# Performance work log

Measured on AMD Instinct MI355X. Metric: run time of the kernel, lower is better.

## Reference

```python
import jax, jax.numpy as jnp
import numpy as np

B, N, EMB, HID, CODE, FEAT, L = 8, 96, 768, 384, 192, 768, 2
NEG = 1e30  # mask_logic constant


def _gru(x, h, Wih, Whh, bih, bhh):
    # torch.nn.GRUCell math; gate order r, z, n
    gi = x @ Wih.T + bih
    gh = h @ Whh.T + bhh
    ir, iz, inn = jnp.split(gi, 3, axis=-1)
    hr, hz, hn = jnp.split(gh, 3, axis=-1)
    r = jax.nn.sigmoid(ir + hr)
    z = jax.nn.sigmoid(iz + hz)
    n = jnp.tanh(inn + r * hn)
    return (1.0 - z) * n + z * h


def _node0(Hl, gc, gp):
    # node 0: C = gru_c(x, 0); P = gru_p(0, x); H1 = C + P
    x0 = Hl[:, 0]
    z0 = jnp.zeros_like(x0)
    h0 = _gru(x0, z0, *gc) + _gru(z0, x0, *gp)
    b, n, d = Hl.shape
    return jnp.zeros((b, n, d), Hl.dtype).at[:, 0].set(h0)


def _dag_scan(Hl, s_mask, aux, Wr0, Wr1, gc, gp, get_w):
    # sequential DAG recurrence: node i attends over nodes < i of the CURRENT layer's outputs
    b, n, d = Hl.shape
    buf0 = _node0(Hl, gc, gp)
    pos = jnp.arange(n)

    def step(buf, inp):
        i, q, s_row, aux_row = inp
        valid = pos < i                                  # growing history slice [:i]
        w = get_w(buf, q, aux_row, valid)                # (B,N), zero for j >= i
        s = s_row[:, :, None]
        V = (buf @ Wr0.T) * s + (buf @ Wr1.T) * (1.0 - s)  # speaker-relation values
        M = jnp.einsum('bn,bnd->bd', w, V)
        hn = _gru(q, M, *gc) + _gru(M, q, *gp)           # C + P
        return buf.at[:, i].set(hn), w

    xs = (jnp.arange(1, n),
          jnp.swapaxes(Hl[:, 1:], 0, 1),
          jnp.swapaxes(s_mask[:, 1:], 0, 1),
          jnp.swapaxes(aux[:, 1:], 0, 1))
    buf, ws = jax.lax.scan(step, buf0, xs)
    return buf, jnp.swapaxes(ws, 0, 1)  # H1 (B,N,D), attn rows 1..N-1 (B,N-1,N)


def _mlp(x, W0, b0, W1, b1):
    # out_mlp with mlp_layers=1 (dropout is identity in eval mode)
    return jax.nn.relu(x @ W0.T + b0) @ W1.T + b1


def _forward(features, adj, s_mask, s_mask_onehot,
             enc_fc1_W, enc_fc1_b, enc_gat_w, enc_gat_b, enc_Wr0, enc_Wr1,
             enc_gruc_Wih, enc_gruc_Whh, enc_gruc_bih, enc_gruc_bhh,
             enc_grup_Wih, enc_grup_Whh, enc_grup_bih, enc_grup_bhh,
             enc_mlp_W0, enc_mlp_b0, enc_mlp_W1, enc_mlp_b1,
             dec_fc1_W, dec_fc1_b, dec_Wr0, dec_Wr1,
             dec_gruc_Wih, dec_gruc_Whh, dec_gruc_bih, dec_gruc_bhh,
             dec_grup_Wih, dec_grup_Whh, dec_grup_bih, dec_grup_bhh,
             dec_mlp_W0, dec_mlp_b0, dec_mlp_W1, dec_mlp_b1,
             lengths):
    b, n, _ = features.shape
    I = jnp.broadcast_to(jnp.eye(n, dtype=features.dtype), (b, n, n))
    # ----- encoder -----
    Hs = [jax.nn.relu(features @ enc_fc1_W.T + enc_fc1_b)]
    adjB_list = [jnp.zeros((b, 1, n), features.dtype)]
    for l in range(L):
        gc = (enc_gruc_Wih[l], enc_gruc_Whh[l], enc_gruc_bih[l], enc_gruc_bhh[l])
        gp = (enc_grup_Wih[l], enc_grup_Whh[l], enc_grup_bih[l], enc_grup_bhh[l])
        wq, wk, gb = enc_gat_w[l, :HID], enc_gat_w[l, HID:], enc_gat_b[l]

        def get_w(buf, q, adj_row, valid, wq=wq, wk=wk, gb=gb):
            # GAT_encoder: alpha = Linear([q; K]) masked by adj over history (mask_logic)
            alpha = buf @ wk + (q @ wq)[:, None] + gb
            alpha = alpha - (1.0 - adj_row) * NEG
            alpha = jnp.where(valid[None, :], alpha, -jnp.inf)
            return jax.nn.softmax(alpha, axis=-1)

        H1, ws = _dag_scan(Hs[l], s_mask, adj, enc_Wr0[l], enc_Wr1[l], gc, gp, get_w)
        Hs.append(H1)
        # row 0 of adjB is zeros; rows 1..N-1 are zero-padded attention weights
        adjB_list.append(jnp.concatenate([jnp.zeros((b, 1, n), features.dtype), ws], axis=1))
    fU = _mlp(jnp.concatenate(Hs, axis=-1), enc_mlp_W0, enc_mlp_b0, enc_mlp_W1, enc_mlp_b1)
    # ----- decoder -----
    Hs = [jax.nn.relu(fU @ dec_fc1_W.T + dec_fc1_b)]
    for l in range(L):
        gc = (dec_gruc_Wih[l], dec_gruc_Whh[l], dec_gruc_bih[l], dec_gruc_bhh[l])
        gp = (dec_grup_Wih[l], dec_grup_Whh[l], dec_grup_bih[l], dec_grup_bhh[l])
        b_inv = jnp.linalg.solve(I, I - adjB_list[l + 1])

        def get_w(buf, q, w_row, valid):
            # GNN_decoder: uses b_inv[:, i, :i] directly as gather weights
            return jnp.where(valid[None, :], w_row, 0.0)

        H1, _ = _dag_scan(Hs[l], s_mask, b_inv, dec_Wr0[l], dec_Wr1[l], gc, gp, get_w)
        Hs.append(H1)
    logits = _mlp(jnp.concatenate(Hs, axis=-1), dec_mlp_W0, dec_mlp_b0, dec_mlp_W1, dec_mlp_b1)
    feature_map = jnp.linalg.solve(I, I - adjB_list[2])
    return logits, feature_map


def setup_inputs() -> dict:
    key = jax.random.key(0)
    ks = iter(jax.random.split(key, 48))

    def rn(*shape):
        return jax.random.normal(next(ks), shape, jnp.float32) * 0.05

    return dict(
        features=jax.random.normal(next(ks), (B, N, EMB), jnp.float32),
        adj=jax.random.randint(next(ks), (B, N, N), 0, 2).astype(jnp.float32),
        s_mask=jax.random.randint(next(ks), (B, N, N), 0, 2).astype(jnp.float32),
        s_mask_onehot=jnp.zeros((B, N, N, 2), jnp.float32),
        lengths=jax.random.randint(next(ks), (B,), 1, N),
        enc_fc1_W=rn(HID, EMB), enc_fc1_b=rn(HID),
        enc_gat_w=rn(L, 2 * HID), enc_gat_b=rn(L),
        enc_Wr0=rn(L, HID, HID), enc_Wr1=rn(L, HID, HID),
        enc_gruc_Wih=rn(L, 3 * HID, HID), enc_gruc_Whh=rn(L, 3 * HID, HID),
        enc_gruc_bih=rn(L, 3 * HID), enc_gruc_bhh=rn(L, 3 * HID),
        enc_grup_Wih=rn(L, 3 * HID, HID), enc_grup_Whh=rn(L, 3 * HID, HID),
        enc_grup_bih=rn(L, 3 * HID), enc_grup_bhh=rn(L, 3 * HID),
        enc_mlp_W0=rn(HID, (L + 1) * HID), enc_mlp_b0=rn(HID),
        enc_mlp_W1=rn(CODE, HID), enc_mlp_b1=rn(CODE),
        dec_fc1_W=rn(HID, CODE), dec_fc1_b=rn(HID),
        dec_Wr0=rn(L, HID, HID), dec_Wr1=rn(L, HID, HID),
        dec_gruc_Wih=rn(L, 3 * HID, HID), dec_gruc_Whh=rn(L, 3 * HID, HID),
        dec_gruc_bih=rn(L, 3 * HID), dec_gruc_bhh=rn(L, 3 * HID),
        dec_grup_Wih=rn(L, 3 * HID, HID), dec_grup_Whh=rn(L, 3 * HID, HID),
        dec_grup_bih=rn(L, 3 * HID), dec_grup_bhh=rn(L, 3 * HID),
        dec_mlp_W0=rn(HID, (L + 1) * HID), dec_mlp_b0=rn(HID),
        dec_mlp_W1=rn(FEAT, HID), dec_mlp_b1=rn(FEAT),
    )


def reference(features, adj, s_mask, s_mask_onehot, lengths,
              enc_fc1_W, enc_fc1_b, enc_gat_w, enc_gat_b, enc_Wr0, enc_Wr1,
              enc_gruc_Wih, enc_gruc_Whh, enc_gruc_bih, enc_gruc_bhh,
              enc_grup_Wih, enc_grup_Whh, enc_grup_bih, enc_grup_bhh,
              enc_mlp_W0, enc_mlp_b0, enc_mlp_W1, enc_mlp_b1,
              dec_fc1_W, dec_fc1_b, dec_Wr0, dec_Wr1,
              dec_gruc_Wih, dec_gruc_Whh, dec_gruc_bih, dec_gruc_bhh,
              dec_grup_Wih, dec_grup_Whh, dec_grup_bih, dec_grup_bhh,
              dec_mlp_W0, dec_mlp_b0, dec_mlp_W1, dec_mlp_b1):
    return _forward(features, adj, s_mask, s_mask_onehot,
                    enc_fc1_W, enc_fc1_b, enc_gat_w, enc_gat_b, enc_Wr0, enc_Wr1,
                    enc_gruc_Wih, enc_gruc_Whh, enc_gruc_bih, enc_gruc_bhh,
                    enc_grup_Wih, enc_grup_Whh, enc_grup_bih, enc_grup_bhh,
                    enc_mlp_W0, enc_mlp_b0, enc_mlp_W1, enc_mlp_b1,
                    dec_fc1_W, dec_fc1_b, dec_Wr0, dec_Wr1,
                    dec_gruc_Wih, dec_gruc_Whh, dec_gruc_bih, dec_gruc_bhh,
                    dec_grup_Wih, dec_grup_Whh, dec_grup_bih, dec_grup_bhh,
                    dec_mlp_W0, dec_mlp_b0, dec_mlp_W1, dec_mlp_b1,
                    lengths)
```

## Files before the change

kernel.cpp:

```cpp
#include <hip/hip_runtime.h>
#include <math.h>

#define B_    8
#define N_    96
#define EMB_  768
#define HID_  384
#define GID_  1152
#define CONC_ 1152
#define CODE_ 192
#define FEAT_ 768
#define NSL_  64
#define SD_   6
#define NRW_  42

__device__ __forceinline__ float sigf(float x) { return 1.0f / (1.0f + expf(-x)); }

__device__ __forceinline__ void atstf(float* p, float v) {
  __hip_atomic_store(p, v, __ATOMIC_RELAXED, __HIP_MEMORY_SCOPE_AGENT);
}
__device__ __forceinline__ float atldf(const float* p) {
  return __hip_atomic_load((float*)p, __ATOMIC_RELAXED, __HIP_MEMORY_SCOPE_AGENT);
}
__device__ __forceinline__ float dot4(float4 a, float4 b) {
  return fmaf(a.x, b.x, fmaf(a.y, b.y, fmaf(a.z, b.z, a.w * b.w)));
}

template<int RELU>
__global__ __launch_bounds__(256)
void gemm_bias(const float* __restrict__ A, int lda,
               const float* __restrict__ W,
               const float* __restrict__ bias,
               float* __restrict__ C, int ldc, int K)
{
  __shared__ float As[16][68];
  __shared__ float Bs[16][68];
  const int tid = threadIdx.x;
  const int m0 = blockIdx.y * 64;
  const int n0 = blockIdx.x * 64;
  const int lr = tid >> 2;
  const int lc = (tid & 3) * 4;
  const int ty = tid >> 4, tx = tid & 15;
  float acc[4][4] = {};
  for (int k0 = 0; k0 < K; k0 += 16) {
    float4 a4 = *(const float4*)(A + (size_t)(m0 + lr) * lda + k0 + lc);
    float4 b4 = *(const float4*)(W + (size_t)(n0 + lr) * K + k0 + lc);
    As[lc+0][lr] = a4.x; As[lc+1][lr] = a4.y; As[lc+2][lr] = a4.z; As[lc+3][lr] = a4.w;
    Bs[lc+0][lr] = b4.x; Bs[lc+1][lr] = b4.y; Bs[lc+2][lr] = b4.z; Bs[lc+3][lr] = b4.w;
    __syncthreads();
#pragma unroll
    for (int k = 0; k < 16; ++k) {
      float av[4], bv[4];
#pragma unroll
      for (int i = 0; i < 4; ++i) av[i] = As[k][ty*4+i];
#pragma unroll
      for (int j = 0; j < 4; ++j) bv[j] = Bs[k][tx*4+j];
#pragma unroll
      for (int i = 0; i < 4; ++i)
#pragma unroll
        for (int j = 0; j < 4; ++j) acc[i][j] = fmaf(av[i], bv[j], acc[i][j]);
    }
    __syncthreads();
  }
#pragma unroll
  for (int i = 0; i < 4; ++i) {
    int m = m0 + ty*4 + i;
#pragma unroll
    for (int j = 0; j < 4; ++j) {
      int n = n0 + tx*4 + j;
      float v = acc[i][j] + bias[n];
      if (RELU) v = fmaxf(v, 0.0f);
      C[(size_t)m * ldc + n] = v;
    }
  }
}

__global__ __launch_bounds__(256)
void prod_kernel(const float* __restrict__ Ac, const float* __restrict__ Ap,
                 const float* __restrict__ W0, const float* __restrict__ W1,
                 float* __restrict__ G)
{
  const float* A = (blockIdx.z < 2) ? Ac : Ap;
  const float* W = (blockIdx.z & 1) ? W1 : W0;
  float* C = G + (size_t)blockIdx.z * GID_ * HID_;
  __shared__ float As[16][68];
  __shared__ float Bs[16][68];
  const int tid = threadIdx.x;
  const int m0 = blockIdx.y * 64;
  const int n0 = blockIdx.x * 64;
  const int lr = tid >> 2;
  const int lc = (tid & 3) * 4;
  const int lr2 = tid & 63, kq = tid >> 6;
  const int ty = tid >> 4, tx = tid & 15;
  float acc[4][4] = {};
  for (int k0 = 0; k0 < HID_; k0 += 16) {
    float4 a4 = *(const float4*)(A + (size_t)(m0 + lr) * HID_ + k0 + lc);
    As[lc+0][lr] = a4.x; As[lc+1][lr] = a4.y; As[lc+2][lr] = a4.z; As[lc+3][lr] = a4.w;
#pragma unroll
    for (int u = 0; u < 4; ++u) {
      int kl = kq * 4 + u;
      Bs[kl][lr2] = W[(size_t)(k0 + kl) * HID_ + n0 + lr2];
    }
    __syncthreads();
#pragma unroll
    for (int k = 0; k < 16; ++k) {
      float av[4], bv[4];
#pragma unroll
      for (int i = 0; i < 4; ++i) av[i] = As[k][ty*4+i];
#pragma unroll
      for (int j = 0; j < 4; ++j) bv[j] = Bs[k][tx*4+j];
#pragma unroll
      for (int i = 0; i < 4; ++i)
#pragma unroll
        for (int j = 0; j < 4; ++j) acc[i][j] = fmaf(av[i], bv[j], acc[i][j]);
    }
    __syncthreads();
  }
#pragma unroll
  for (int i = 0; i < 4; ++i)
#pragma unroll
    for (int j = 0; j < 4; ++j)
      C[(size_t)(m0 + ty*4 + i) * HID_ + n0 + tx*4 + j] = acc[i][j];
}

struct ScanP {
  const float* Hl;
  float*       bufC;
  float*       hnX;
  const float* G;
  const float* GIc;
  const float* GHp;
  const float* bhhc;
  const float* bihp;
  const float* Wr0;
  const float* Wr1;
  const float* wk;
  const float* mask;
  const float* smask;
  float*       adjB;
};

template<int ENC>
__global__ __launch_bounds__(256, 2)
void scan_kernel(ScanP p)
{
  const int tid  = threadIdx.x;
  const int b    = blockIdx.x >> 6;
  const int sl   = blockIdx.x & 63;
  const int j0   = sl * SD_;
  const int team = tid >> 4, lane = tid & 15;

  __shared__ __align__(16) float stage[HID_];
  __shared__ float ws0[N_], ws1[N_], s_sm[N_];
  __shared__ float alpha[N_];
  __shared__ float dots[48];
  __shared__ float red4[4];
  __shared__ float sh_aknew;
  __shared__ float PA[NRW_ * 97];
  __shared__ float PB[NRW_ * 97];

  for (int k = tid; k < NRW_ * 97; k += 256) { PA[k] = 0.f; PB[k] = 0.f; }

  float4 wAr[3][6], wBr[3][6];
#pragma unroll
  for (int u = 0; u < 3; ++u) {
    const int r = team + 16 * u;
    const float *Aptr, *Bptr;
    if (r < 36) {
      const int g = r / 6, jl = r % 6;
      const size_t off = (size_t)((g % 3) * HID_ + j0 + jl) * HID_;
      const float* base = p.G + (g < 3 ? 0 : 2) * (size_t)GID_ * HID_;
      Aptr = base + off;
      Bptr = base + (size_t)GID_ * HID_ + off;
    } else if (r < 42) {
      const int jl = r - 36;
      Aptr = p.Wr0 + (size_t)(j0 + jl) * HID_;
      Bptr = p.Wr1 + (size_t)(j0 + jl) * HID_;
    } else if (r == 42 && ENC) {
      Aptr = p.wk; Bptr = p.wk;
    } else {
      Aptr = p.Wr0; Bptr = p.Wr1;
    }
#pragma unroll
    for (int m = 0; m < 6; ++m) {
      wAr[u][m] = ((const float4*)Aptr)[lane + 16*m];
      wBr[u][m] = ((const float4*)Bptr)[lane + 16*m];
    }
  }
  float bh0=0, bh1=0, bh2=0, bi0=0, bi1=0, bi2=0;
  if (tid < SD_) {
    int j = j0 + tid;
    bh0 = p.bhhc[j]; bh1 = p.bhhc[HID_ + j]; bh2 = p.bhhc[2*HID_ + j];
    bi0 = p.bihp[j]; bi1 = p.bihp[HID_ + j]; bi2 = p.bihp[2*HID_ + j];
  }

#define BULK_STAGE(SRC)                                                      \
  do {                                                                       \
    if (tid < NSL_) {                                                        \
      const float* f_ = (SRC) + tid * SD_;                                   \
      while (__float_as_uint(atldf(f_)) == 0xFFFFFFFFu) {}                   \
    }                                                                        \
    __syncthreads();                                                         \
    {                                                                        \
      float v0 = atldf((SRC) + tid);                                         \
      while (__float_as_uint(v0) == 0xFFFFFFFFu) v0 = atldf((SRC) + tid);    \
      stage[tid] = v0;                                                       \
      if (tid < HID_ - 256) {                                                \
        float v1 = atldf((SRC) + 256 + tid);                                 \
        while (__float_as_uint(v1) == 0xFFFFFFFFu)                           \
          v1 = atldf((SRC) + 256 + tid);                                     \
        stage[256 + tid] = v1;                                               \
      }                                                                      \
    }                                                                        \
    __syncthreads();                                                         \
  } while (0)

  if (tid < SD_) {
    int j = j0 + tid;
    const float* gi = p.GIc + (size_t)(b * N_) * GID_;
    const float* gh = p.GHp + (size_t)(b * N_) * GID_;
    float rc = sigf(gi[j] + bh0);
    float zc = sigf(gi[HID_ + j] + bh1);
    float nc = tanhf(gi[2*HID_ + j] + rc * bh2);
    float outc = (1.0f - zc) * nc;
    float rp = sigf(bi0 + gh[j]);
    float zp = sigf(bi1 + gh[HID_ + j]);
    float np = tanhf(bi2 + rp * gh[2*HID_ + j]);
    float x0 = p.Hl[(size_t)(b * N_) * CONC_ + j];
    float h0 = outc + (1.0f - zp) * np + zp * x0;
    p.bufC[(size_t)(b * N_) * CONC_ + j] = h0;
    atstf(&p.hnX[(size_t)(b * N_) * HID_ + j], h0);
  }
  __syncthreads();

  for (int i = 1; i < N_; ++i) {
    float pf_gi0=0, pf_gi1=0, pf_gi2=0, pf_gh0=0, pf_gh1=0, pf_gh2=0, pf_q=0;
    if (tid < SD_) {
      int j = j0 + tid;
      const float* gi = p.GIc + ((size_t)b * N_ + i) * GID_;
      const float* gh = p.GHp + ((size_t)b * N_ + i) * GID_;
      pf_gi0 = gi[j]; pf_gi1 = gi[HID_ + j]; pf_gi2 = gi[2*HID_ + j];
      pf_gh0 = gh[j]; pf_gh1 = gh[HID_ + j]; pf_gh2 = gh[2*HID_ + j];
      pf_q   = p.Hl[((size_t)b * N_ + i) * CONC_ + j];
    }
    float pf_mrow = 0.0f;
    if (tid < N_) {
      pf_mrow = p.mask[((size_t)b * N_ + i) * N_ + tid];
      s_sm[tid] = p.smask[((size_t)b * N_ + i) * N_ + tid];
    }

    const float* srcH = p.hnX + (size_t)(b * N_ + (i - 1)) * HID_;
    BULK_STAGE(srcH);
    const float4* st4 = (const float4*)stage;
    float4 hreg[6];
#pragma unroll
    for (int m = 0; m < 6; ++m) hreg[m] = st4[lane + 16*m];

#pragma unroll
    for (int u = 0; u < 3; ++u) {
      const int r = team + 16 * u;
      float a = 0.f, bv = 0.f;
#pragma unroll
      for (int m = 0; m < 6; ++m) {
        a  += dot4(wAr[u][m], hreg[m]);
        bv += dot4(wBr[u][m], hreg[m]);
      }
#pragma unroll
      for (int mm = 8; mm; mm >>= 1) {
        a  += __shfl_xor(a, mm);
        bv += __shfl_xor(bv, mm);
      }
      if (lane == 0) {
        if (r < NRW_) { PA[r * 97 + (i - 1)] = a; PB[r * 97 + (i - 1)] = bv; }
        else if (ENC && r == 42) sh_aknew = a;
      }
    }
    __syncthreads();

    if (ENC) {
      if (tid == 0) alpha[i - 1] = sh_aknew;
      float av = -3.0e38f;
      if (tid < i) {
        float ak = (tid == i - 1) ? sh_aknew : alpha[tid];
        av = ak - (1.0f - pf_mrow) * 1e30f;
      }
      float v = av;
#pragma unroll
      for (int m = 32; m; m >>= 1) v = fmaxf(v, __shfl_xor(v, m));
      if ((tid & 63) == 0) red4[tid >> 6] = v;
      __syncthreads();
      float mx = fmaxf(fmaxf(red4[0], red4[1]), fmaxf(red4[2], red4[3]));
      __syncthreads();
      float e = (tid < i) ? expf(av - mx) : 0.0f;
      v = e;
#pragma unroll
      for (int m = 32; m; m >>= 1) v += __shfl_xor(v, m);
      if ((tid & 63) == 0) red4[tid >> 6] = v;
      __syncthreads();
      float ssum = red4[0] + red4[1] + red4[2] + red4[3];
      if (tid < N_) {
        float w = (tid < i) ? e / ssum : 0.0f;
        float sv = s_sm[tid];
        ws0[tid] = w * sv;
        ws1[tid] = w - w * sv;
        if (sl == 0) p.adjB[((size_t)b * N_ + i) * N_ + tid] = w;
      }
      __syncthreads();
    } else {
      if (tid < N_) {
        float w = (tid < i) ? -pf_mrow : 0.0f;
        float sv = s_sm[tid];
        ws0[tid] = w * sv;
        ws1[tid] = w - w * sv;
      }
      __syncthreads();
    }

    {
      float wsr0[6], wsr1[6];
#pragma unroll
      for (int k = 0; k < 6; ++k) {
        wsr0[k] = ws0[lane + 16*k];
        wsr1[k] = ws1[lane + 16*k];
      }
#pragma unroll
      for (int u = 0; u < 3; ++u) {
        const int r = team + 16 * u;
        if (r < NRW_) {
          float acc = 0.f;
#pragma unroll
          for (int k = 0; k < 6; ++k) {
            int n = lane + 16*k;
            acc = fmaf(wsr0[k], PA[r * 97 + n], fmaf(wsr1[k], PB[r * 97 + n], acc));
          }
#pragma unroll
          for (int mm = 8; mm; mm >>= 1) acc += __shfl_xor(acc, mm);
          if (lane == 0) dots[r] = acc;
        }
      }
    }
    __syncthreads();

    if (tid < SD_) {
      int j = j0 + tid;
      float Mj = dots[36 + tid];
      float rc = sigf(pf_gi0 + dots[tid] + bh0);
      float zc = sigf(pf_gi1 + dots[6 + tid] + bh1);
      float nc = tanhf(pf_gi2 + rc * (dots[12 + tid] + bh2));
      float outc = (1.0f - zc) * nc + zc * Mj;
      float rp = sigf(dots[18 + tid] + bi0 + pf_gh0);
      float zp = sigf(dots[24 + tid] + bi1 + pf_gh1);
      float np = tanhf(dots[30 + tid] + bi2 + rp * pf_gh2);
      float hv = outc + (1.0f - zp) * np + zp * pf_q;
      p.bufC[((size_t)b * N_ + i) * CONC_ + j] = hv;
      atstf(&p.hnX[((size_t)b * N_ + i) * HID_ + j], hv);
    }
    __syncthreads();
  }
#undef BULK_STAGE
}

__global__ __launch_bounds__(256)
void fmap_kernel(const float* __restrict__ adjB2, float* __restrict__ out)
{
  int idx = blockIdx.x * 256 + threadIdx.x;
  if (idx < B_ * N_ * N_) {
    int j = idx % N_;
    int i = (idx / N_) % N_;
    float a = (i == 0) ? 0.0f : adjB2[idx];
    out[idx] = ((i == j) ? 1.0f : 0.0f) - a;
  }
}

extern "C" void kernel_launch(void* const* d_in, const int* in_sizes, int n_in,
                              void* d_out, int out_size, void* d_ws, size_t ws_size,
                              hipStream_t stream)
{
  (void)in_sizes; (void)n_in; (void)out_size; (void)ws_size;
  const float* features     = (const float*)d_in[0];
  const float* adj          = (const float*)d_in[1];
  const float* s_mask       = (const float*)d_in[2];
  const float* enc_fc1_W    = (const float*)d_in[5];
  const float* enc_fc1_b    = (const float*)d_in[6];
  const float* enc_gat_w    = (const float*)d_in[7];
  const float* enc_Wr0      = (const float*)d_in[9];
  const float* enc_Wr1      = (const float*)d_in[10];
  const float* enc_gruc_Wih = (const float*)d_in[11];
  const float* enc_gruc_Whh = (const float*)d_in[12];
  const float* enc_gruc_bih = (const float*)d_in[13];
  const float* enc_gruc_bhh = (const float*)d_in[14];
  const float* enc_grup_Wih = (const float*)d_in[15];
  const float* enc_grup_Whh = (const float*)d_in[16];
  const float* enc_grup_bih = (const float*)d_in[17];
  const float* enc_grup_bhh = (const float*)d_in[18];
  const float* enc_mlp_W0   = (const float*)d_in[19];
  const float* enc_mlp_b0   = (const float*)d_in[20];
  const float* enc_mlp_W1   = (const float*)d_in[21];
  const float* enc_mlp_b1   = (const float*)d_in[22];
  const float* dec_fc1_W    = (const float*)d_in[23];
  const float* dec_fc1_b    = (const float*)d_in[24];
  const float* dec_Wr0      = (const float*)d_in[25];
  const float* dec_Wr1      = (const float*)d_in[26];
  const float* dec_gruc_Wih = (const float*)d_in[27];
  const float* dec_gruc_Whh = (const float*)d_in[28];
  const float* dec_gruc_bih = (const float*)d_in[29];
  const float* dec_gruc_bhh = (const float*)d_in[30];
  const float* dec_grup_Wih = (const float*)d_in[31];
  const float* dec_grup_Whh = (const float*)d_in[32];
  const float* dec_grup_bih = (const float*)d_in[33];
  const float* dec_grup_bhh = (const float*)d_in[34];
  const float* dec_mlp_W0   = (const float*)d_in[35];
  const float* dec_mlp_b0   = (const float*)d_in[36];
  const float* dec_mlp_W1   = (const float*)d_in[37];
  const float* dec_mlp_b1   = (const float*)d_in[38];

  float* ws = (float*)d_ws;
  size_t o = 0;
  float* Hse   = ws + o; o += (size_t)B_ * N_ * CONC_;
  float* Hsd   = ws + o; o += (size_t)B_ * N_ * CONC_;
  float* GIc   = ws + o; o += (size_t)B_ * N_ * GID_;
  float* GHp   = ws + o; o += (size_t)B_ * N_ * GID_;
  float* adjB1 = ws + o; o += (size_t)B_ * N_ * N_;
  float* adjB2 = ws + o; o += (size_t)B_ * N_ * N_;
  float* fU    = ws + o; o += (size_t)B_ * N_ * CODE_;
  float* Tmp   = ws + o; o += (size_t)B_ * N_ * HID_;
  float* hnX   = ws + o; o += (size_t)B_ * N_ * HID_;
  float* Gbuf  = ws + o; o += (size_t)4 * GID_ * HID_;
  const size_t hn_bytes = (size_t)B_ * N_ * HID_ * sizeof(float);

  const dim3 blk(256);
  float* logits = (float*)d_out;
  float* fmap   = (float*)d_out + (size_t)B_ * N_ * FEAT_;

  gemm_bias<1><<<dim3(6, 12), blk, 0, stream>>>(features, EMB_, enc_fc1_W, enc_fc1_b,
                                                Hse, CONC_, EMB_);
  for (int l = 0; l < 2; ++l) {
    const float* Hl = Hse + l * HID_;
    gemm_bias<0><<<dim3(18, 12), blk, 0, stream>>>(Hl, CONC_,
        enc_gruc_Wih + (size_t)l * GID_ * HID_, enc_gruc_bih + l * GID_, GIc, GID_, HID_);
    gemm_bias<0><<<dim3(18, 12), blk, 0, stream>>>(Hl, CONC_,
        enc_grup_Whh + (size_t)l * GID_ * HID_, enc_grup_bhh + l * GID_, GHp, GID_, HID_);
    prod_kernel<<<dim3(6, 18, 4), blk, 0, stream>>>(
        enc_gruc_Whh + (size_t)l * GID_ * HID_, enc_grup_Wih + (size_t)l * GID_ * HID_,
        enc_Wr0 + (size_t)l * HID_ * HID_, enc_Wr1 + (size_t)l * HID_ * HID_, Gbuf);
    hipMemsetAsync(hnX, 0xFF, hn_bytes, stream);
    ScanP p;
    p.Hl = Hl; p.bufC = Hse + (l + 1) * HID_;
    p.hnX = hnX; p.G = Gbuf;
    p.GIc = GIc; p.GHp = GHp;
    p.bhhc = enc_gruc_bhh + l * GID_;
    p.bihp = enc_grup_bih + l * GID_;
    p.Wr0 = enc_Wr0 + (size_t)l * HID_ * HID_;
    p.Wr1 = enc_Wr1 + (size_t)l * HID_ * HID_;
    p.wk = enc_gat_w + l * 2 * HID_ + HID_;
    p.mask = adj; p.smask = s_mask;
    p.adjB = (l == 0) ? adjB1 : adjB2;
    scan_kernel<1><<<dim3(512), blk, 0, stream>>>(p);
  }
  gemm_bias<1><<<dim3(6, 12), blk, 0, stream>>>(Hse, CONC_, enc_mlp_W0, enc_mlp_b0,
                                                Tmp, HID_, CONC_);
  gemm_bias<0><<<dim3(3, 12), blk, 0, stream>>>(Tmp, HID_, enc_mlp_W1, enc_mlp_b1,
                                                fU, CODE_, HID_);
  gemm_bias<1><<<dim3(6, 12), blk, 0, stream>>>(fU, CODE_, dec_fc1_W, dec_fc1_b,
                                                Hsd, CONC_, CODE_);
  for (int l = 0; l < 2; ++l) {
    const float* Hl = Hsd + l * HID_;
    gemm_bias<0><<<dim3(18, 12), blk, 0, stream>>>(Hl, CONC_,
        dec_gruc_Wih + (size_t)l * GID_ * HID_, dec_gruc_bih + l * GID_, GIc, GID_, HID_);
    gemm_bias<0><<<dim3(18, 12), blk, 0, stream>>>(Hl, CONC_,
        dec_grup_Whh + (size_t)l * GID_ * HID_, dec_grup_bhh + l * GID_, GHp, GID_, HID_);
    prod_kernel<<<dim3(6, 18, 4), blk, 0, stream>>>(
        dec_gruc_Whh + (size_t)l * GID_ * HID_, dec_grup_Wih + (size_t)l * GID_ * HID_,
        dec_Wr0 + (size_t)l * HID_ * HID_, dec_Wr1 + (size_t)l * HID_ * HID_, Gbuf);
    hipMemsetAsync(hnX, 0xFF, hn_bytes, stream);
    ScanP p;
    p.Hl = Hl; p.bufC = Hsd + (l + 1) * HID_;
    p.hnX = hnX; p.G = Gbuf;
    p.GIc = GIc; p.GHp = GHp;
    p.bhhc = dec_gruc_bhh + l * GID_;
    p.bihp = dec_grup_bih + l * GID_;
    p.Wr0 = dec_Wr0 + (size_t)l * HID_ * HID_;
    p.Wr1 = dec_Wr1 + (size_t)l * HID_ * HID_;
    p.wk = nullptr;
    p.mask = (l == 0) ? adjB1 : adjB2;
    p.smask = s_mask;
    p.adjB = nullptr;
    scan_kernel<0><<<dim3(512), blk, 0, stream>>>(p);
  }
  gemm_bias<1><<<dim3(6, 12), blk, 0, stream>>>(Hsd, CONC_, dec_mlp_W0, dec_mlp_b0,
                                                Tmp, HID_, CONC_);
  gemm_bias<0><<<dim3(12, 12), blk, 0, stream>>>(Tmp, HID_, dec_mlp_W1, dec_mlp_b1,
                                                 logits, FEAT_, HID_);
  fmap_kernel<<<dim3((B_ * N_ * N_ + 255) / 256), blk, 0, stream>>>(adjB2, fmap);
}
```

Measured before the change: 1.961 ms.

## Precompute partial softmax and history dot before waiting on the newest node

The scan step is restructured so the softmax over the already known history and the weighted PA/PB reduction run before the wait for node i-1's hidden state. The newest entry is then folded in with an online-softmax rescale from the freshly computed projections. This takes that work off the cross-block dependency chain. The change also drops the flag-polling phase in favour of direct spin loads with s_sleep, remaps block indices so slices are spread across the grid, and pins weight registers with inline asm. The risks are numerical differences from the online rescale, extra register pressure, and correctness of the remapping, which depends on the grid size.

```diff
diff --git a/kernel.cpp b/kernel.cpp
--- a/kernel.cpp
+++ b/kernel.cpp
@@ -24,6 +24,7 @@
 __device__ __forceinline__ float dot4(float4 a, float4 b) {
   return fmaf(a.x, b.x, fmaf(a.y, b.y, fmaf(a.z, b.z, a.w * b.w)));
 }
+#define PIN4(v4) asm volatile("" : "+v"((v4).x), "+v"((v4).y), "+v"((v4).z), "+v"((v4).w))
 
 template<int RELU>
 __global__ __launch_bounds__(256)
@@ -144,16 +145,17 @@
 void scan_kernel(ScanP p)
 {
   const int tid  = threadIdx.x;
-  const int b    = blockIdx.x >> 6;
-  const int sl   = blockIdx.x & 63;
+  const int bid  = blockIdx.x;
+  const int b    = (bid >> 3) & 7;
+  const int sl   = ((bid & 7) << 3) | (bid >> 6);
   const int j0   = sl * SD_;
   const int team = tid >> 4, lane = tid & 15;
 
   __shared__ __align__(16) float stage[HID_];
-  __shared__ float ws0[N_], ws1[N_], s_sm[N_];
+  __shared__ float Ew0[N_], Ew1[N_], s_sm[N_], msk[N_];
   __shared__ float alpha[N_];
   __shared__ float dots[48];
-  __shared__ float red4[4];
+  __shared__ float red4a[4], red4b[4];
   __shared__ float sh_aknew;
   __shared__ float PA[NRW_ * 97];
   __shared__ float PB[NRW_ * 97];
@@ -186,6 +188,11 @@
       wBr[u][m] = ((const float4*)Bptr)[lane + 16*m];
     }
   }
+#pragma unroll
+  for (int u = 0; u < 3; ++u)
+#pragma unroll
+    for (int m = 0; m < 6; ++m) { PIN4(wAr[u][m]); PIN4(wBr[u][m]); }
+
   float bh0=0, bh1=0, bh2=0, bi0=0, bi1=0, bi2=0;
   if (tid < SD_) {
     int j = j0 + tid;
@@ -195,21 +202,19 @@
 
 #define BULK_STAGE(SRC)                                                      \
   do {                                                                       \
-    if (tid < NSL_) {                                                        \
-      const float* f_ = (SRC) + tid * SD_;                                   \
-      while (__float_as_uint(atldf(f_)) == 0xFFFFFFFFu) {}                   \
+    float v0 = atldf((SRC) + tid);                                           \
+    while (__float_as_uint(v0) == 0xFFFFFFFFu) {                             \
+      __builtin_amdgcn_s_sleep(2);                                           \
+      v0 = atldf((SRC) + tid);                                               \
     }                                                                        \
-    __syncthreads();                                                         \
-    {                                                                        \
-      float v0 = atldf((SRC) + tid);                                         \
-      while (__float_as_uint(v0) == 0xFFFFFFFFu) v0 = atldf((SRC) + tid);    \
-      stage[tid] = v0;                                                       \
-      if (tid < HID_ - 256) {                                                \
-        float v1 = atldf((SRC) + 256 + tid);                                 \
-        while (__float_as_uint(v1) == 0xFFFFFFFFu)                           \
-          v1 = atldf((SRC) + 256 + tid);                                     \
-        stage[256 + tid] = v1;                                               \
+    stage[tid] = v0;                                                         \
+    if (tid < HID_ - 256) {                                                  \
+      float v1 = atldf((SRC) + 256 + tid);                                   \
+      while (__float_as_uint(v1) == 0xFFFFFFFFu) {                           \
+        __builtin_amdgcn_s_sleep(2);                                         \
+        v1 = atldf((SRC) + 256 + tid);                                       \
       }                                                                      \
+      stage[256 + tid] = v1;                                                 \
     }                                                                        \
     __syncthreads();                                                         \
   } while (0)
@@ -242,10 +247,59 @@
       pf_gh0 = gh[j]; pf_gh1 = gh[HID_ + j]; pf_gh2 = gh[2*HID_ + j];
       pf_q   = p.Hl[((size_t)b * N_ + i) * CONC_ + j];
     }
-    float pf_mrow = 0.0f;
+    float mr = 0.f, sv_ = 0.f;
     if (tid < N_) {
-      pf_mrow = p.mask[((size_t)b * N_ + i) * N_ + tid];
-      s_sm[tid] = p.smask[((size_t)b * N_ + i) * N_ + tid];
+      mr  = p.mask[((size_t)b * N_ + i) * N_ + tid];
+      sv_ = p.smask[((size_t)b * N_ + i) * N_ + tid];
+      msk[tid] = mr; s_sm[tid] = sv_;
+    }
+    float f_mx = 0.f, f_se = 0.f;
+    if (ENC) {
+      float av = -3.0e38f;
+      if (tid < i - 1) av = alpha[tid] - (1.0f - mr) * 1e30f;
+      float v = av;
+#pragma unroll
+      for (int m = 32; m; m >>= 1) v = fmaxf(v, __shfl_xor(v, m));
+      if ((tid & 63) == 0) red4a[tid >> 6] = v;
+      __syncthreads();
+      f_mx = fmaxf(fmaxf(red4a[0], red4a[1]), fmaxf(red4a[2], red4a[3]));
+      float e = (tid < i - 1) ? expf(av - f_mx) : 0.0f;
+      v = e;
+#pragma unroll
+      for (int m = 32; m; m >>= 1) v += __shfl_xor(v, m);
+      if ((tid & 63) == 0) red4b[tid >> 6] = v;
+      if (tid < N_) { Ew0[tid] = e * sv_; Ew1[tid] = e - e * sv_; }
+      __syncthreads();
+      f_se = red4b[0] + red4b[1] + red4b[2] + red4b[3];
+    } else {
+      if (tid < N_) {
+        float w = (tid < i - 1) ? -mr : 0.0f;
+        Ew0[tid] = w * sv_; Ew1[tid] = w - w * sv_;
+      }
+      __syncthreads();
+    }
+
+    float er0[6], er1[6];
+#pragma unroll
+    for (int k = 0; k < 6; ++k) {
+      er0[k] = Ew0[lane + 16*k];
+      er1[k] = Ew1[lane + 16*k];
+    }
+    float sa_keep[3] = {0.f, 0.f, 0.f};
+#pragma unroll
+    for (int u = 0; u < 3; ++u) {
+      const int r = team + 16 * u;
+      if (r < NRW_) {
+        float acc = 0.f;
+#pragma unroll
+        for (int k = 0; k < 6; ++k) {
+          int n = lane + 16*k;
+          acc = fmaf(er0[k], PA[r * 97 + n], fmaf(er1[k], PB[r * 97 + n], acc));
+        }
+#pragma unroll
+        for (int mm = 8; mm; mm >>= 1) acc += __shfl_xor(acc, mm);
+        sa_keep[u] = acc;
+      }
     }
 
     const float* srcH = p.hnX + (size_t)(b * N_ + (i - 1)) * HID_;
@@ -255,6 +309,7 @@
 #pragma unroll
     for (int m = 0; m < 6; ++m) hreg[m] = st4[lane + 16*m];
 
+    float a_keep[3], b_keep[3];
 #pragma unroll
     for (int u = 0; u < 3; ++u) {
       const int r = team + 16 * u;
@@ -269,6 +324,7 @@
         a  += __shfl_xor(a, mm);
         bv += __shfl_xor(bv, mm);
       }
+      a_keep[u] = a; b_keep[u] = bv;
       if (lane == 0) {
         if (r < NRW_) { PA[r * 97 + (i - 1)] = a; PB[r * 97 + (i - 1)] = bv; }
         else if (ENC && r == 42) sh_aknew = a;
@@ -276,68 +332,26 @@
     }
     __syncthreads();
 
+    float c_scale, c_elast, c_inv;
     if (ENC) {
-      if (tid == 0) alpha[i - 1] = sh_aknew;
-      float av = -3.0e38f;
-      if (tid < i) {
-        float ak = (tid == i - 1) ? sh_aknew : alpha[tid];
-        av = ak - (1.0f - pf_mrow) * 1e30f;
-      }
-      float v = av;
-#pragma unroll
-      for (int m = 32; m; m >>= 1) v = fmaxf(v, __shfl_xor(v, m));
-      if ((tid & 63) == 0) red4[tid >> 6] = v;
-      __syncthreads();
-      float mx = fmaxf(fmaxf(red4[0], red4[1]), fmaxf(red4[2], red4[3]));
-      __syncthreads();
-      float e = (tid < i) ? expf(av - mx) : 0.0f;
-      v = e;
-#pragma unroll
-      for (int m = 32; m; m >>= 1) v += __shfl_xor(v, m);
-      if ((tid & 63) == 0) red4[tid >> 6] = v;
-      __syncthreads();
-      float ssum = red4[0] + red4[1] + red4[2] + red4[3];
-      if (tid < N_) {
-        float w = (tid < i) ? e / ssum : 0.0f;
-        float sv = s_sm[tid];
-        ws0[tid] = w * sv;
-        ws1[tid] = w - w * sv;
-        if (sl == 0) p.adjB[((size_t)b * N_ + i) * N_ + tid] = w;
-      }
-      __syncthreads();
+      float av_last = sh_aknew - (1.0f - msk[i - 1]) * 1e30f;
+      float m_new = fmaxf(f_mx, av_last);
+      c_scale = expf(f_mx - m_new);
+      c_elast = expf(av_last - m_new);
+      c_inv = 1.0f / (f_se * c_scale + c_elast);
     } else {
-      if (tid < N_) {
-        float w = (tid < i) ? -pf_mrow : 0.0f;
-        float sv = s_sm[tid];
-        ws0[tid] = w * sv;
-        ws1[tid] = w - w * sv;
-      }
-      __syncthreads();
-    }
-
-    {
-      float wsr0[6], wsr1[6];
-#pragma unroll
-      for (int k = 0; k < 6; ++k) {
-        wsr0[k] = ws0[lane + 16*k];
-        wsr1[k] = ws1[lane + 16*k];
-      }
-#pragma unroll
-      for (int u = 0; u < 3; ++u) {
-        const int r = team + 16 * u;
-        if (r < NRW_) {
-          float acc = 0.f;
-#pragma unroll
-          for (int k = 0; k < 6; ++k) {
-            int n = lane + 16*k;
-            acc = fmaf(wsr0[k], PA[r * 97 + n], fmaf(wsr1[k], PB[r * 97 + n], acc));
-          }
-#pragma unroll
-          for (int mm = 8; mm; mm >>= 1) acc += __shfl_xor(acc, mm);
-          if (lane == 0) dots[r] = acc;
-        }
-      }
-    }
+      c_scale = 1.0f; c_elast = -msk[i - 1]; c_inv = 1.0f;
+    }
+    float s_last = s_sm[i - 1];
+#pragma unroll
+    for (int u = 0; u < 3; ++u) {
+      const int r = team + 16 * u;
+      if (r < NRW_ && lane == 0)
+        dots[r] = (sa_keep[u] * c_scale
+                   + c_elast * (s_last * a_keep[u] + (1.0f - s_last) * b_keep[u]))
+                  * c_inv;
+    }
+    if (ENC && tid == 0) alpha[i - 1] = sh_aknew;
     __syncthreads();
 
     if (tid < SD_) {
@@ -353,6 +367,13 @@
       float hv = outc + (1.0f - zp) * np + zp * pf_q;
       p.bufC[((size_t)b * N_ + i) * CONC_ + j] = hv;
       atstf(&p.hnX[((size_t)b * N_ + i) * HID_ + j], hv);
+    }
+    if (ENC && sl == 0 && tid < N_) {
+      float w;
+      if (tid < i - 1)      w = (Ew0[tid] + Ew1[tid]) * c_scale * c_inv;
+      else if (tid == i - 1) w = c_elast * c_inv;
+      else                   w = 0.0f;
+      p.adjB[((size_t)b * N_ + i) * N_ + tid] = w;
     }
     __syncthreads();
   }
```

New measurement: 2.279 ms. 16.2% more time.
